# Kernel tuning notes

Measured on AMD Instinct MI355X. Metric: run time of the kernel, lower is better.

Reference implementation:

```python
import jax, jax.numpy as jnp
import numpy as np

B, L, C, H, FF = 2, 2048, 1024, 16, 4096
HD = C // H
SCALE = HD ** -0.5
EPS = 1e-5


def _ln(x, g, b):
    m = jnp.mean(x, axis=-1, keepdims=True)
    v = jnp.mean((x - m) ** 2, axis=-1, keepdims=True)
    return (x - m) * jax.lax.rsqrt(v + EPS) * g + b


def setup_inputs() -> dict:
    key = jax.random.key(0)
    ks = jax.random.split(key, 12)
    s = lambda fan_in: 1.0 / np.sqrt(fan_in)
    return {
        "x": jax.random.normal(ks[0], (B, L, C), jnp.float32),
        "freq_diff": jax.random.normal(ks[1], (B, L), jnp.float32),
        "qkv_w": jax.random.normal(ks[2], (C, 3 * C), jnp.float32) * s(C),
        "qkv_b": jnp.zeros((3 * C,), jnp.float32),
        "fp_w1": jax.random.normal(ks[3], (1, C), jnp.float32),
        "fp_b1": jnp.zeros((C,), jnp.float32),
        "fp_ln_g": jnp.ones((C,), jnp.float32),
        "fp_ln_b": jnp.zeros((C,), jnp.float32),
        "fp_w2": jax.random.normal(ks[4], (C, C), jnp.float32) * s(C),
        "fp_b2": jnp.zeros((C,), jnp.float32),
        "wq_w": jax.random.normal(ks[5], (HD, HD), jnp.float32) * s(HD),
        "wq_b": jnp.zeros((HD,), jnp.float32),
        "wk_w": jax.random.normal(ks[6], (HD, HD), jnp.float32) * s(HD),
        "wk_b": jnp.zeros((HD,), jnp.float32),
        "out_w": jax.random.normal(ks[7], (C, C), jnp.float32) * s(C),
        "out_b": jnp.zeros((C,), jnp.float32),
        "n1_g": jnp.ones((C,), jnp.float32),
        "n1_b": jnp.zeros((C,), jnp.float32),
        "n2_g": jnp.ones((C,), jnp.float32),
        "n2_b": jnp.zeros((C,), jnp.float32),
        "mlp_w1": jax.random.normal(ks[8], (C, FF), jnp.float32) * s(C),
        "mlp_b1": jnp.zeros((FF,), jnp.float32),
        "mlp_w2": jax.random.normal(ks[9], (FF, C), jnp.float32) * s(FF),
        "mlp_b2": jnp.zeros((C,), jnp.float32),
        "freq_scale": jnp.ones((1,), jnp.float32),
    }


def reference(x, freq_diff, qkv_w, qkv_b, fp_w1, fp_b1, fp_ln_g, fp_ln_b,
              fp_w2, fp_b2, wq_w, wq_b, wk_w, wk_b, out_w, out_b,
              n1_g, n1_b, n2_g, n2_b, mlp_w1, mlp_b1, mlp_w2, mlp_b2,
              freq_scale):
    shortcut = x
    xn = _ln(x, n1_g, n1_b)
    qkv = (xn @ qkv_w + qkv_b).reshape(B, L, 3, H, HD)
    qkv = jnp.transpose(qkv, (2, 0, 3, 1, 4))  # [3,B,H,L,HD]
    q, k, v = qkv[0], qkv[1], qkv[2]

    # frequency bias: MLP on scalar freq_diff -> per-head bias vectors
    fb = freq_diff[..., None] @ fp_w1 + fp_b1          # [B,L,C]
    fb = jax.nn.gelu(_ln(fb, fp_ln_g, fp_ln_b), approximate=False)
    fb = fb @ fp_w2 + fp_b2                            # [B,L,C]
    fb = jnp.transpose(fb.reshape(B, L, H, HD), (0, 2, 1, 3))  # [B,H,L,HD]
    qb = fb @ wq_w + wq_b
    kb = fb @ wk_w + wk_b
    freq_attn_bias = jnp.einsum('bhqd,bhkd->bhqk', qb, kb)

    attn = jnp.einsum('bhqd,bhkd->bhqk', q, k) * SCALE
    attn = attn + freq_scale[0] * freq_attn_bias
    attn = jax.nn.softmax(attn, axis=-1)
    o = jnp.einsum('bhqk,bhkd->bhqd', attn, v)
    o = jnp.transpose(o, (0, 2, 1, 3)).reshape(B, L, C)
    x = shortcut + (o @ out_w + out_b)

    xn2 = _ln(x, n2_g, n2_b)
    h = jax.nn.gelu(xn2 @ mlp_w1 + mlp_b1, approximate=False)
    x = x + (h @ mlp_w2 + mlp_b2)
    return x
```

## Files before the change

### kernel.cpp

```cpp
#include <hip/hip_runtime.h>
#include <math.h>


typedef __bf16 bf16;
typedef float f32x4 __attribute__((ext_vector_type(4)));
typedef bf16 bf16x8 __attribute__((ext_vector_type(8)));
typedef bf16 bf16x4 __attribute__((ext_vector_type(4)));

#define DEVINL __device__ __forceinline__

#define LOG2E 1.4426950408889634f

DEVINL float fast_exp2(float x) { return __builtin_amdgcn_exp2f(x); }

DEVINL void async_load16(const void* g, void* l) {
  __builtin_amdgcn_global_load_lds(
      (const __attribute__((address_space(1))) unsigned int*)g,
      (__attribute__((address_space(3))) unsigned int*)l, 16, 0, 0);
}

DEVINL f32x4 mfma16(bf16x8 a, bf16x8 b, f32x4 c) {
  return __builtin_amdgcn_mfma_f32_16x16x32_bf16(a, b, c, 0, 0, 0);
}

DEVINL float gelu_exact(float v) {
  return 0.5f * v * (1.0f + erff(v * 0.70710678118654752f));
}

DEVINL void hard_barrier() {
  asm volatile("" ::: "memory");
  __builtin_amdgcn_s_barrier();
  asm volatile("" ::: "memory");
}

DEVINL void block_reduce2(float& a, float& b, float* red, int tid) {
#pragma unroll
  for (int off = 32; off >= 1; off >>= 1) {
    a += __shfl_xor(a, off);
    b += __shfl_xor(b, off);
  }
  int w = tid >> 6;
  if ((tid & 63) == 0) { red[2 * w] = a; red[2 * w + 1] = b; }
  __syncthreads();
  a = red[0] + red[2] + red[4] + red[6];
  b = red[1] + red[3] + red[5] + red[7];
  __syncthreads();
}

__global__ __launch_bounds__(256) void pre_kernel(
    const float* __restrict__ qkv_w, const float* __restrict__ out_w,
    const float* __restrict__ mlp_w1, const float* __restrict__ mlp_w2,
    bf16* __restrict__ qkv_wt, bf16* __restrict__ out_wt,
    bf16* __restrict__ w1t, bf16* __restrict__ w2t,
    const float* __restrict__ x, const float* __restrict__ fd,
    const float* __restrict__ g1, const float* __restrict__ b1,
    const float* __restrict__ fw1, const float* __restrict__ fb1,
    const float* __restrict__ flg, const float* __restrict__ flb,
    bf16* __restrict__ xn, bf16* __restrict__ gout) {
  __shared__ float tile[32][33];
  __shared__ float red[8];
  const int id = blockIdx.x, t = threadIdx.x;
  if (id < 12288) {
    const float* W; bf16* Wt; int K, N, bx, by;
    if (id < 3072) {
      W = qkv_w; Wt = qkv_wt; K = 1024; N = 3072; bx = id % 96; by = id / 96;
    } else if (id < 4096) {
      int i = id - 3072;
      W = out_w; Wt = out_wt; K = 1024; N = 1024; bx = i & 31; by = i >> 5;
    } else if (id < 8192) {
      int i = id - 4096;
      W = mlp_w1; Wt = w1t; K = 1024; N = 4096; bx = i & 127; by = i >> 7;
    } else {
      int i = id - 8192;
      W = mlp_w2; Wt = w2t; K = 4096; N = 1024; bx = i & 31; by = i >> 5;
    }
    int n0 = bx * 32, k0 = by * 32;
    int tx = t & 31, ty = t >> 5;
#pragma unroll
    for (int r = 0; r < 4; ++r)
      tile[ty + r * 8][tx] = W[(size_t)(k0 + ty + r * 8) * N + n0 + tx];
    __syncthreads();
#pragma unroll
    for (int r = 0; r < 4; ++r)
      Wt[(size_t)(n0 + ty + r * 8) * K + k0 + tx] = (bf16)tile[tx][ty + r * 8];
    return;
  }
  int tok = id - 12288;
  float4 xv = ((const float4*)(x + (size_t)tok * 1024))[t];
  float s = xv.x + xv.y + xv.z + xv.w;
  float ss = xv.x * xv.x + xv.y * xv.y + xv.z * xv.z + xv.w * xv.w;
  block_reduce2(s, ss, red, t);
  float mean = s * (1.0f / 1024.0f);
  float rsig = rsqrtf(ss * (1.0f / 1024.0f) - mean * mean + 1e-5f);
  float4 g4 = ((const float4*)g1)[t], b4 = ((const float4*)b1)[t];
  bf16x4 o;
  o[0] = (bf16)((xv.x - mean) * rsig * g4.x + b4.x);
  o[1] = (bf16)((xv.y - mean) * rsig * g4.y + b4.y);
  o[2] = (bf16)((xv.z - mean) * rsig * g4.z + b4.z);
  o[3] = (bf16)((xv.w - mean) * rsig * g4.w + b4.w);
  ((bf16x4*)xn)[(size_t)tok * 256 + t] = o;

  float dv = fd[tok];
  float4 w4 = ((const float4*)fw1)[t], c4 = ((const float4*)fb1)[t];
  float f0 = dv * w4.x + c4.x, f1 = dv * w4.y + c4.y;
  float f2 = dv * w4.z + c4.z, f3 = dv * w4.w + c4.w;
  s = f0 + f1 + f2 + f3;
  ss = f0 * f0 + f1 * f1 + f2 * f2 + f3 * f3;
  block_reduce2(s, ss, red, t);
  mean = s * (1.0f / 1024.0f);
  rsig = rsqrtf(ss * (1.0f / 1024.0f) - mean * mean + 1e-5f);
  float4 lg = ((const float4*)flg)[t], lb = ((const float4*)flb)[t];
  bf16x4 q;
  q[0] = (bf16)gelu_exact((f0 - mean) * rsig * lg.x + lb.x);
  q[1] = (bf16)gelu_exact((f1 - mean) * rsig * lg.y + lb.y);
  q[2] = (bf16)gelu_exact((f2 - mean) * rsig * lg.z + lb.z);
  q[3] = (bf16)gelu_exact((f3 - mean) * rsig * lg.w + lb.w);
  ((bf16x4*)gout)[(size_t)tok * 256 + t] = q;
}

__global__ __launch_bounds__(256) void prec_qk(
    const float* __restrict__ fp_w2, const float* __restrict__ fp_b2,
    const float* __restrict__ wq_w, const float* __restrict__ wq_b,
    const float* __restrict__ wk_w, const float* __restrict__ wk_b,
    bf16* __restrict__ wqk2t, float* __restrict__ bqk) {
  __shared__ float Wl[64 * 64];
  __shared__ float Al[64 * 128];
  const int id = blockIdx.x;
  const int sel = id >> 7, h = (id >> 3) & 15, ck = id & 7;
  const int t = threadIdx.x;
  const float* wsel = sel ? wk_w : wq_w;
#pragma unroll
  for (int i = 0; i < 4; ++i)
    ((float4*)Wl)[i * 256 + t] = ((const float4*)wsel)[i * 256 + t];
  const int c0 = ck * 128, off = h * 64;
#pragma unroll
  for (int it = 0; it < 8; ++it) {
    int idx = it * 256 + t;
    int rr = idx >> 4, c4 = idx & 15;
    float4 v = *(const float4*)(fp_w2 + (size_t)(c0 + rr) * 1024 + off + c4 * 4);
    float vv[4] = {v.x, v.y, v.z, v.w};
#pragma unroll
    for (int k = 0; k < 4; ++k) {
      int i2 = c4 * 4 + k;
      Al[i2 * 128 + (rr ^ (i2 & 31))] = vv[k];
    }
  }
  __syncthreads();
  const int cr = t & 127, jh = (t >> 7) * 32;
  float acc[32];
#pragma unroll
  for (int j = 0; j < 32; ++j) acc[j] = 0.f;
  for (int i = 0; i < 64; ++i) {
    float a = Al[i * 128 + (cr ^ (i & 31))];
    const float4* wrow = (const float4*)(Wl + i * 64 + jh);
#pragma unroll
    for (int j4 = 0; j4 < 8; ++j4) {
      float4 wv = wrow[j4];
      acc[j4 * 4 + 0] += a * wv.x;
      acc[j4 * 4 + 1] += a * wv.y;
      acc[j4 * 4 + 2] += a * wv.z;
      acc[j4 * 4 + 3] += a * wv.w;
    }
  }
  const int nbase = sel * 1024 + off + jh;
#pragma unroll
  for (int j = 0; j < 32; ++j)
    wqk2t[(size_t)(nbase + j) * 1024 + c0 + cr] = (bf16)acc[j];
  if (ck == 0 && t < 64) {
    float s = 0.f;
    for (int i = 0; i < 64; ++i) s += fp_b2[off + i] * Wl[i * 64 + t];
    bqk[sel * 1024 + off + t] = s + (sel ? wk_b[t] : wq_b[t]);
  }
}

__global__ __launch_bounds__(256) void ln_kernel(
    const float* __restrict__ xin, const float* __restrict__ g,
    const float* __restrict__ b, bf16* __restrict__ xout) {
  __shared__ float red[8];
  int tok = blockIdx.x, t = threadIdx.x;
  float4 xv = ((const float4*)(xin + (size_t)tok * 1024))[t];
  float s = xv.x + xv.y + xv.z + xv.w;
  float ss = xv.x * xv.x + xv.y * xv.y + xv.z * xv.z + xv.w * xv.w;
  block_reduce2(s, ss, red, t);
  float mean = s * (1.0f / 1024.0f);
  float rsig = rsqrtf(ss * (1.0f / 1024.0f) - mean * mean + 1e-5f);
  float4 g4 = ((const float4*)g)[t], b4 = ((const float4*)b)[t];
  bf16x4 o;
  o[0] = (bf16)((xv.x - mean) * rsig * g4.x + b4.x);
  o[1] = (bf16)((xv.y - mean) * rsig * g4.y + b4.y);
  o[2] = (bf16)((xv.z - mean) * rsig * g4.z + b4.z);
  o[3] = (bf16)((xv.w - mean) * rsig * g4.w + b4.w);
  ((bf16x4*)xout)[(size_t)tok * 256 + t] = o;
}

#define PHASE(MH, NH, LA, LB, STAGE_STMT, WAIT_STMT)                          \
  do {                                                                        \
    if (LA) {                                                                 \
      _Pragma("unroll") for (int ml = 0; ml < 4; ++ml) {                      \
        _Pragma("unroll") for (int ks = 0; ks < 2; ++ks) {                    \
          const int rr = ml * 16 + lm;                                        \
          const int cc = (((ks * 4 + quad) ^ (lm & 7)) << 3);                 \
          af[ml][ks] = *(const bf16x8*)&As[bsel][MH][wm][rr][cc];             \
        }                                                                     \
      }                                                                       \
    }                                                                         \
    if (LB) {                                                                 \
      _Pragma("unroll") for (int nl = 0; nl < 2; ++nl) {                      \
        _Pragma("unroll") for (int ks = 0; ks < 2; ++ks) {                    \
          const int rr = nl * 16 + lm;                                        \
          const int cc = (((ks * 4 + quad) ^ (lm & 7)) << 3);                 \
          bfr[nl][ks] = *(const bf16x8*)&Bs[bsel][NH][wn][rr][cc];            \
        }                                                                     \
      }                                                                       \
    }                                                                         \
    STAGE_STMT;                                                               \
    WAIT_STMT;                                                                \
    hard_barrier();                                                           \
    __builtin_amdgcn_s_setprio(1);                                            \
    _Pragma("unroll") for (int ks = 0; ks < 2; ++ks) {                        \
      _Pragma("unroll") for (int ml = 0; ml < 4; ++ml) {                      \
        _Pragma("unroll") for (int nl = 0; nl < 2; ++nl) {                    \
          acc[(MH)*4 + ml][(NH)*2 + nl] = mfma16(                             \
              af[ml][ks], bfr[nl][ks], acc[(MH)*4 + ml][(NH)*2 + nl]);        \
        }                                                                     \
      }                                                                       \
    }                                                                         \
    __builtin_amdgcn_s_setprio(0);                                            \
  } while (0)

template <class Epi>
__global__ __launch_bounds__(512, 2) void gemm256(
    const bf16* __restrict__ A, const bf16* __restrict__ Bt,
    int lda, int ldb, int K, int kstride, int nbx, int nblk, int rowoffz,
    Epi epi) {
  __shared__ __align__(16) bf16 As[2][2][2][64][64];
  __shared__ __align__(16) bf16 Bs[2][2][4][32][64];

  const int tid = threadIdx.x;
  const int lane = tid & 63, w = tid >> 6;
  const int quad = lane >> 4, lm = lane & 15;
  const int wm = w >> 2, wn = w & 3;

  const int kz = blockIdx.x / nblk;
  const int bid = blockIdx.x - kz * nblk;
  const int swz = (nblk & 7) ? bid : ((bid & 7) * (nblk >> 3) + (bid >> 3));
  const int tm = swz / nbx, tn = swz - tm * nbx;
  const int m0 = tm << 8, n0 = tn << 8;
  const int rowoff = kz * rowoffz;
  A += (size_t)kz * kstride;
  Bt += (size_t)kz * kstride;

  const bf16* Abase = A + (size_t)m0 * lda;
  const bf16* Bbase = Bt + (size_t)n0 * ldb;

  auto stageA = [&](int b, int mh, int kt) {
#pragma unroll
    for (int j = 0; j < 2; ++j) {
      const int q = (w * 2 + j) * 64 + lane;
      const int wm2 = q >> 9, rr = (q >> 3) & 63, c = q & 7;
      async_load16(Abase + (size_t)(wm2 * 128 + mh * 64 + rr) * lda +
                       (size_t)kt * 64 + ((c ^ (rr & 7)) << 3),
                   (char*)&As[b][mh][0][0][0] + (w * 2 + j) * 1024);
    }
  };
  auto stageB = [&](int b, int nh, int kt) {
#pragma unroll
    for (int j = 0; j < 2; ++j) {
      const int q = (w * 2 + j) * 64 + lane;
      const int wn4 = q >> 8, rr = (q >> 3) & 31, c = q & 7;
      async_load16(Bbase + (size_t)(wn4 * 64 + nh * 32 + rr) * ldb +
                       (size_t)kt * 64 + ((c ^ (rr & 7)) << 3),
                   (char*)&Bs[b][nh][0][0][0] + (w * 2 + j) * 1024);
    }
  };

  f32x4 acc[8][4];
#pragma unroll
  for (int i = 0; i < 8; ++i)
#pragma unroll
    for (int j = 0; j < 4; ++j) {
      acc[i][j][0] = 0.f; acc[i][j][1] = 0.f;
      acc[i][j][2] = 0.f; acc[i][j][3] = 0.f;
    }
  bf16x8 af[4][2], bfr[2][2];

  stageA(0, 0, 0);
  stageB(0, 1, 0);
  stageA(0, 1, 0);
  stageB(0, 0, 0);
  stageA(1, 0, 1);
  stageB(1, 1, 1);
  asm volatile("s_waitcnt vmcnt(4)" ::: "memory");
  hard_barrier();

  const int nt = K >> 6;
  int bsel = 0;
  for (int t = 0; t < nt; ++t, bsel ^= 1) {
    PHASE(0, 0, 1, 1, { if (t + 1 < nt) stageA(bsel ^ 1, 1, t + 1); }, {});
    PHASE(0, 1, 0, 1, { if (t + 1 < nt) stageB(bsel ^ 1, 0, t + 1); }, {});
    PHASE(1, 1, 1, 0, { if (t + 2 < nt) stageA(bsel, 0, t + 2); }, {});
    PHASE(1, 0, 0, 1, { if (t + 2 < nt) stageB(bsel, 1, t + 2); },
          {
            if (t + 2 < nt) {
              asm volatile("s_waitcnt vmcnt(4)" ::: "memory");
            } else if (t + 1 < nt) {
              asm volatile("s_waitcnt vmcnt(0)" ::: "memory");
            }
          });
  }

#pragma unroll
  for (int mi = 0; mi < 8; ++mi)
#pragma unroll
    for (int ni = 0; ni < 4; ++ni)
      epi(rowoff + m0 + wm * 128 + mi * 16 + quad * 4,
          n0 + wn * 64 + ni * 16 + lm, acc[mi][ni]);
}

template <class Epi>
__global__ __launch_bounds__(256) void gemm_bf16_k(
    const bf16* __restrict__ A, const bf16* __restrict__ Bt,
    int M, int N, int K, Epi epi) {
  __shared__ bf16 As[2][128 * 32];
  __shared__ bf16 Bs[2][128 * 32];
  const int tid = threadIdx.x;
  const int lane = tid & 63, w = tid >> 6;
  const int quad = lane >> 4, lm = lane & 15;
  const int wm = w >> 1, wn = w & 1;
  const int m0 = blockIdx.y * 128, n0 = blockIdx.x * 128;

  f32x4 acc[4][4];
#pragma unroll
  for (int i = 0; i < 4; ++i)
#pragma unroll
    for (int j = 0; j < 4; ++j) {
      acc[i][j][0] = 0.f; acc[i][j][1] = 0.f; acc[i][j][2] = 0.f; acc[i][j][3] = 0.f;
    }

  const bf16* Ag = A + (size_t)m0 * K;
  const bf16* Bg = Bt + (size_t)n0 * K;

  auto stage = [&](int k0, int buf) {
#pragma unroll
    for (int i = 0; i < 2; ++i) {
      int ch = i * 256 + tid, r = ch >> 2, c = ch & 3;
      async_load16(Ag + (size_t)r * K + k0 + c * 8,
                   (char*)As[buf] + (i * 256 + w * 64) * 16);
      async_load16(Bg + (size_t)r * K + k0 + c * 8,
                   (char*)Bs[buf] + (i * 256 + w * 64) * 16);
    }
  };

  stage(0, 0);
  const int nk = K >> 5;
  for (int ki = 0; ki < nk; ++ki) {
    __syncthreads();
    if (ki + 1 < nk) stage((ki + 1) << 5, (ki + 1) & 1);
    const bf16* Ac = As[ki & 1];
    const bf16* Bc = Bs[ki & 1];
    bf16x8 af[4], bfv[4];
#pragma unroll
    for (int mi = 0; mi < 4; ++mi)
      af[mi] = *(const bf16x8*)(Ac + (wm * 64 + mi * 16 + lm) * 32 + quad * 8);
#pragma unroll
    for (int ni = 0; ni < 4; ++ni)
      bfv[ni] = *(const bf16x8*)(Bc + (wn * 64 + ni * 16 + lm) * 32 + quad * 8);
#pragma unroll
    for (int mi = 0; mi < 4; ++mi)
#pragma unroll
      for (int ni = 0; ni < 4; ++ni)
        acc[mi][ni] = mfma16(af[mi], bfv[ni], acc[mi][ni]);
  }

#pragma unroll
  for (int mi = 0; mi < 4; ++mi)
#pragma unroll
    for (int ni = 0; ni < 4; ++ni)
      epi(m0 + wm * 64 + mi * 16 + quad * 4, n0 + wn * 64 + ni * 16 + lm, acc[mi][ni]);
}

__global__ __launch_bounds__(256) void reduce_mlp2(
    const float* __restrict__ part, float* __restrict__ out) {
  size_t i = (size_t)blockIdx.x * 256 + threadIdx.x;
  const float4* p = (const float4*)part;
  float4 o = ((const float4*)out)[i];
  const size_t S = (size_t)4096 * 256;
  float4 a = p[i], b = p[i + S], c = p[i + 2 * S], d = p[i + 3 * S];
  o.x += a.x + b.x + c.x + d.x;
  o.y += a.y + b.y + c.y + d.y;
  o.z += a.z + b.z + c.z + d.z;
  o.w += a.w + b.w + c.w + d.w;
  ((float4*)out)[i] = o;
}

struct EpiQKV {
  const float* __restrict__ bias;
  bf16 *Qc, *Kc, *Vt;
  DEVINL void operator()(int row, int col, f32x4 v) const {
    int b = row >> 11, l = row & 2047;
    float bia = bias[col];
    if (col < 1024) {
      int h = col >> 6, d = col & 63;
      bf16* p = Qc + (size_t)(((b << 4) + h) * 2048 + l) * 128 + d;
#pragma unroll
      for (int r = 0; r < 4; ++r) p[r * 128] = (bf16)((v[r] + bia) * (0.125f * LOG2E));
    } else if (col < 2048) {
      int c2 = col - 1024, h = c2 >> 6, d = c2 & 63;
      bf16* p = Kc + (size_t)(((b << 4) + h) * 2048 + l) * 128 + d;
#pragma unroll
      for (int r = 0; r < 4; ++r) p[r * 128] = (bf16)(v[r] + bia);
    } else {
      int c2 = col - 2048, h = c2 >> 6, d = c2 & 63;
      bf16x4 pk;
#pragma unroll
      for (int r = 0; r < 4; ++r) pk[r] = (bf16)(v[r] + bia);
      *(bf16x4*)(Vt + (size_t)(((b << 4) + h) * 64 + d) * 2048 + l) = pk;
    }
  }
};

struct EpiQBKB {
  const float* __restrict__ bias;
  const float* __restrict__ fs;
  bf16 *Qc, *Kc;
  DEVINL void operator()(int row, int col, f32x4 v) const {
    int b = row >> 11, l = row & 2047;
    float bia = bias[col];
    if (col < 1024) {
      int h = col >> 6, d = col & 63;
      float sc = fs[0] * LOG2E;
      bf16* p = Qc + (size_t)(((b << 4) + h) * 2048 + l) * 128 + 64 + d;
#pragma unroll
      for (int r = 0; r < 4; ++r) p[r * 128] = (bf16)((v[r] + bia) * sc);
    } else {
      int c2 = col - 1024, h = c2 >> 6, d = c2 & 63;
      bf16* p = Kc + (size_t)(((b << 4) + h) * 2048 + l) * 128 + 64 + d;
#pragma unroll
      for (int r = 0; r < 4; ++r) p[r * 128] = (bf16)(v[r] + bia);
    }
  }
};

struct EpiOut {
  const float* __restrict__ bias;
  const float* __restrict__ x;
  const float* __restrict__ b2;
  float* x1;
  float* out0;
  DEVINL void operator()(int row, int col, f32x4 v) const {
    float bia = bias[col];
    float b2v = b2[col];
#pragma unroll
    for (int r = 0; r < 4; ++r) {
      size_t idx = (size_t)(row + r) * 1024 + col;
      float xv = x[idx] + v[r] + bia;
      x1[idx] = xv;
      out0[idx] = xv + b2v;
    }
  }
};

struct EpiMLP1 {
  const float* __restrict__ bias;
  bf16* hbf;
  DEVINL void operator()(int row, int col, f32x4 v) const {
    float bia = bias[col];
#pragma unroll
    for (int r = 0; r < 4; ++r)
      hbf[(size_t)(row + r) * 4096 + col] = (bf16)gelu_exact(v[r] + bia);
  }
};

struct EpiPart {
  float* part;
  DEVINL void operator()(int row, int col, f32x4 v) const {
#pragma unroll
    for (int r = 0; r < 4; ++r)
      part[(size_t)(row + r) * 1024 + col] = v[r];
  }
};

__global__ __launch_bounds__(512, 4) void flash_kernel(
    const bf16* __restrict__ Qc, const bf16* __restrict__ Kcp,
    const bf16* __restrict__ Vt, bf16* __restrict__ Obf) {
  __shared__ bf16 KsA[64 * 128];
  __shared__ bf16 KsB[64 * 128];
  __shared__ bf16 VsA[64 * 64];
  __shared__ bf16 VsB[64 * 64];
  __shared__ bf16 Ps[128 * 64];

  const int tid = threadIdx.x, lane = tid & 63, w = tid >> 6;
  const int quad = lane >> 4, lm = lane & 15;
  const int id = blockIdx.x;
  const int bh = id & 31, qt = id >> 5;
  const int b = bh >> 4, h = bh & 15;

  const bf16* Qg = Qc + ((size_t)bh * 2048 + qt * 128) * 128;
#pragma unroll
  for (int i = 0; i < 4; ++i) {
    int ch = i * 512 + tid, r = ch >> 4, cs = ch & 15, c = cs ^ (r & 7);
    char* dst = (i < 2) ? (char*)KsA + (i * 512 + w * 64) * 16
                        : (char*)KsB + ((i - 2) * 512 + w * 64) * 16;
    async_load16(Qg + (size_t)r * 128 + c * 8, dst);
  }
  __syncthreads();
  const int qr = w * 16 + lm;
  bf16x8 qf[4];
  {
    const bf16* base = (w < 4) ? KsA : KsB;
    int rr = qr & 63;
#pragma unroll
    for (int ks = 0; ks < 4; ++ks) {
      int pos = (ks * 4 + quad) ^ (lm & 7);
      qf[ks] = *(const bf16x8*)(base + rr * 128 + pos * 8);
    }
  }
  __syncthreads();

  float m_run = -3.0e38f, l_lane = 0.f;
  f32x4 o_acc[4];
#pragma unroll
  for (int nf = 0; nf < 4; ++nf) {
    o_acc[nf][0] = 0.f; o_acc[nf][1] = 0.f; o_acc[nf][2] = 0.f; o_acc[nf][3] = 0.f;
  }

  const bf16* Kg0 = Kcp + (size_t)bh * 2048 * 128;
  const bf16* Vg0 = Vt + (size_t)bh * 64 * 2048;

  auto stage = [&](int kv, bf16* Kdst, bf16* Vdst) {
    const bf16* Kg = Kg0 + (size_t)kv * 64 * 128;
#pragma unroll
    for (int i = 0; i < 2; ++i) {
      int ch = i * 512 + tid, key = ch >> 4, c = (ch & 15) ^ (key & 7);
      async_load16(Kg + (size_t)key * 128 + c * 8,
                   (char*)Kdst + (i * 512 + w * 64) * 16);
    }
    {
      int d = tid >> 3, c = (tid & 7) ^ (d & 7);
      async_load16(Vg0 + (size_t)d * 2048 + kv * 64 + c * 8,
                   (char*)Vdst + (w * 64) * 16);
    }
  };

  stage(0, KsA, VsA);

  for (int kv = 0; kv < 32; ++kv) {
    const bf16* Kcur = (kv & 1) ? KsB : KsA;
    const bf16* Vcur = (kv & 1) ? VsB : VsA;
    __syncthreads();
    if (kv + 1 < 32)
      stage(kv + 1, (kv & 1) ? KsA : KsB, (kv & 1) ? VsA : VsB);

    f32x4 sa[4];
#pragma unroll
    for (int nk = 0; nk < 4; ++nk) {
      sa[nk][0] = 0.f; sa[nk][1] = 0.f; sa[nk][2] = 0.f; sa[nk][3] = 0.f;
    }
#pragma unroll
    for (int ks = 0; ks < 4; ++ks) {
      bf16x8 ak[4];
#pragma unroll
      for (int nk = 0; nk < 4; ++nk) {
        int key = nk * 16 + lm;
        int pos = (ks * 4 + quad) ^ (key & 7);
        ak[nk] = *(const bf16x8*)(Kcur + key * 128 + pos * 8);
      }
#pragma unroll
      for (int nk = 0; nk < 4; ++nk)
        sa[nk] = mfma16(ak[nk], qf[ks], sa[nk]);
    }

    float mx = fmaxf(fmaxf(sa[0][0], sa[0][1]), sa[0][2]);
    mx = fmaxf(fmaxf(mx, sa[0][3]), sa[1][0]);
    mx = fmaxf(fmaxf(mx, sa[1][1]), sa[1][2]);
    mx = fmaxf(fmaxf(mx, sa[1][3]), sa[2][0]);
    mx = fmaxf(fmaxf(mx, sa[2][1]), sa[2][2]);
    mx = fmaxf(fmaxf(mx, sa[2][3]), sa[3][0]);
    mx = fmaxf(fmaxf(mx, sa[3][1]), sa[3][2]);
    mx = fmaxf(mx, sa[3][3]);
    mx = fmaxf(mx, __shfl_xor(mx, 16));
    mx = fmaxf(mx, __shfl_xor(mx, 32));
    if (__any(mx > m_run + 8.0f)) {
      float mnew = fmaxf(m_run, mx);
      float alpha = fast_exp2(m_run - mnew);
      m_run = mnew;
      l_lane *= alpha;
#pragma unroll
      for (int nf = 0; nf < 4; ++nf) {
        o_acc[nf][0] *= alpha; o_acc[nf][1] *= alpha;
        o_acc[nf][2] *= alpha; o_acc[nf][3] *= alpha;
      }
    }
    float rs = 0.f;
#pragma unroll
    for (int nk = 0; nk < 4; ++nk)
#pragma unroll
      for (int rg = 0; rg < 4; ++rg) {
        float pv = fast_exp2(sa[nk][rg] - m_run);
        sa[nk][rg] = pv;
        rs += pv;
      }
    l_lane += rs;

#pragma unroll
    for (int nk = 0; nk < 4; ++nk) {
      int c16 = 2 * nk + (quad >> 1);
      int cs = c16 ^ (lm & 7);
      bf16x4 pk;
      pk[0] = (bf16)sa[nk][0]; pk[1] = (bf16)sa[nk][1];
      pk[2] = (bf16)sa[nk][2]; pk[3] = (bf16)sa[nk][3];
      *(bf16x4*)(Ps + qr * 64 + cs * 8 + (quad & 1) * 4) = pk;
    }

#pragma unroll
    for (int ks = 0; ks < 2; ++ks) {
      bf16x8 pa, vb[4];
      {
        int cs = (ks * 4 + quad) ^ (lm & 7);
        pa = *(const bf16x8*)(Ps + qr * 64 + cs * 8);
      }
#pragma unroll
      for (int nf = 0; nf < 4; ++nf) {
        int d = nf * 16 + lm;
        int cs = (ks * 4 + quad) ^ (d & 7);
        vb[nf] = *(const bf16x8*)(Vcur + d * 64 + cs * 8);
      }
#pragma unroll
      for (int nf = 0; nf < 4; ++nf)
        o_acc[nf] = mfma16(vb[nf], pa, o_acc[nf]);
    }
  }

  float lt = l_lane;
  lt += __shfl_xor(lt, 16);
  lt += __shfl_xor(lt, 32);
  float inv = 1.0f / lt;
  int l = qt * 128 + qr;
#pragma unroll
  for (int nf = 0; nf < 4; ++nf) {
    bf16x4 ov;
#pragma unroll
    for (int rg = 0; rg < 4; ++rg) ov[rg] = (bf16)(o_acc[nf][rg] * inv);
    int d = h * 64 + nf * 16 + quad * 4;
    *(bf16x4*)(Obf + ((size_t)b * 2048 + l) * 1024 + d) = ov;
  }
}

extern "C" void kernel_launch(void* const* d_in, const int* in_sizes, int n_in,
                              void* d_out, int out_size, void* d_ws, size_t ws_size,
                              hipStream_t stream) {
  (void)in_sizes; (void)n_in; (void)out_size; (void)ws_size;
  const float* x      = (const float*)d_in[0];
  const float* fd     = (const float*)d_in[1];
  const float* qkv_w  = (const float*)d_in[2];
  const float* qkv_b  = (const float*)d_in[3];
  const float* fp_w1  = (const float*)d_in[4];
  const float* fp_b1  = (const float*)d_in[5];
  const float* fp_ln_g= (const float*)d_in[6];
  const float* fp_ln_b= (const float*)d_in[7];
  const float* fp_w2  = (const float*)d_in[8];
  const float* fp_b2  = (const float*)d_in[9];
  const float* wq_w   = (const float*)d_in[10];
  const float* wq_b   = (const float*)d_in[11];
  const float* wk_w   = (const float*)d_in[12];
  const float* wk_b   = (const float*)d_in[13];
  const float* out_w  = (const float*)d_in[14];
  const float* out_b  = (const float*)d_in[15];
  const float* n1_g   = (const float*)d_in[16];
  const float* n1_b   = (const float*)d_in[17];
  const float* n2_g   = (const float*)d_in[18];
  const float* n2_b   = (const float*)d_in[19];
  const float* mlp_w1 = (const float*)d_in[20];
  const float* mlp_b1 = (const float*)d_in[21];
  const float* mlp_w2 = (const float*)d_in[22];
  const float* mlp_b2 = (const float*)d_in[23];
  const float* fscale = (const float*)d_in[24];
  float* out = (float*)d_out;

  char* p = (char*)d_ws;
  auto take = [&](size_t n) { char* r = p; p += (n + 255) & ~(size_t)255; return r; };
  bf16* xn_bf  = (bf16*)take((size_t)4096 * 1024 * 2);
  bf16* g_bf   = (bf16*)take((size_t)4096 * 1024 * 2);
  bf16* Qc     = (bf16*)take((size_t)32 * 2048 * 128 * 2);
  bf16* Kc     = (bf16*)take((size_t)32 * 2048 * 128 * 2);
  bf16* Vt     = (bf16*)take((size_t)32 * 64 * 2048 * 2);
  bf16* o_bf   = (bf16*)take((size_t)4096 * 1024 * 2);
  float* x1    = (float*)take((size_t)4096 * 1024 * 4);
  bf16* ln2_bf = (bf16*)take((size_t)4096 * 1024 * 2);
  bf16* h_bf   = (bf16*)take((size_t)4096 * 4096 * 2);
  bf16* qkv_wt = (bf16*)take((size_t)3072 * 1024 * 2);
  bf16* out_wt = (bf16*)take((size_t)1024 * 1024 * 2);
  bf16* w1t    = (bf16*)take((size_t)4096 * 1024 * 2);
  bf16* w2t    = (bf16*)take((size_t)1024 * 4096 * 2);
  bf16* wqk2t  = (bf16*)take((size_t)2048 * 1024 * 2);
  float* bqk   = (float*)take((size_t)2048 * 4);

  float* part = (float*)xn_bf;

  dim3 b256(256), b512(512);

  prec_qk<<<dim3(256), b256, 0, stream>>>(fp_w2, fp_b2, wq_w, wq_b, wk_w, wk_b, wqk2t, bqk);
  pre_kernel<<<dim3(16384), b256, 0, stream>>>(
      qkv_w, out_w, mlp_w1, mlp_w2, qkv_wt, out_wt, w1t, w2t,
      x, fd, n1_g, n1_b, fp_w1, fp_b1, fp_ln_g, fp_ln_b, xn_bf, g_bf);

  gemm256<<<dim3(192), b512, 0, stream>>>(xn_bf, qkv_wt, 1024, 1024, 1024, 0,
                                          12, 192, 0, EpiQKV{qkv_b, Qc, Kc, Vt});
  gemm256<<<dim3(128), b512, 0, stream>>>(g_bf, wqk2t, 1024, 1024, 1024, 0,
                                          8, 128, 0, EpiQBKB{bqk, fscale, Qc, Kc});
  flash_kernel<<<dim3(512), dim3(512), 0, stream>>>(Qc, Kc, Vt, o_bf);

  gemm_bf16_k<<<dim3(8, 32), b256, 0, stream>>>(o_bf, out_wt, 4096, 1024, 1024,
                                                EpiOut{out_b, x, mlp_b2, x1, out});
  ln_kernel<<<dim3(4096), b256, 0, stream>>>(x1, n2_g, n2_b, ln2_bf);
  gemm256<<<dim3(256), b512, 0, stream>>>(ln2_bf, w1t, 1024, 1024, 1024, 0,
                                          16, 256, 0, EpiMLP1{mlp_b1, h_bf});
  gemm256<<<dim3(256), b512, 0, stream>>>(h_bf, w2t, 4096, 4096, 1024, 1024,
                                          4, 64, 4096, EpiPart{part});
  reduce_mlp2<<<dim3(4096), b256, 0, stream>>>(part, out);
}
```

Measured before the change: 460.8 us.

## Split-K out-proj with gemm256, fuse residual+LN2 reduce, load V directly to registers

The output projection moves from the small 128x128 gemm to the larger gemm256 kernel using a two-way split-K into a partial buffer that reuses the h_bf workspace. A new reduce_oln kernel sums the partials with the residual and bias, writes out0, and computes LayerNorm2 in one pass, replacing the separate epilogue and ln_kernel and dropping the x1 buffer. Separately, the flash kernel stops staging V through LDS and loads V fragments straight from global memory into registers. This cuts LDS use and a pass over memory, at the cost of extra partial-buffer traffic and uncoalesced, unhidden V loads inside the attention loop.

```diff
diff --git a/kernel.cpp b/kernel.cpp
--- a/kernel.cpp
+++ b/kernel.cpp
@@ -173,24 +173,39 @@
   }
 }
 
-__global__ __launch_bounds__(256) void ln_kernel(
-    const float* __restrict__ xin, const float* __restrict__ g,
-    const float* __restrict__ b, bf16* __restrict__ xout) {
+__global__ __launch_bounds__(256) void reduce_oln(
+    const float* __restrict__ part, const float* __restrict__ x,
+    const float* __restrict__ outb, const float* __restrict__ b2,
+    const float* __restrict__ g, const float* __restrict__ bb,
+    float* __restrict__ out0, bf16* __restrict__ ln2) {
   __shared__ float red[8];
   int tok = blockIdx.x, t = threadIdx.x;
-  float4 xv = ((const float4*)(xin + (size_t)tok * 1024))[t];
-  float s = xv.x + xv.y + xv.z + xv.w;
-  float ss = xv.x * xv.x + xv.y * xv.y + xv.z * xv.z + xv.w * xv.w;
+  size_t base = (size_t)tok * 256 + t;
+  const size_t S = (size_t)4096 * 256;
+  float4 p0 = ((const float4*)part)[base];
+  float4 p1 = ((const float4*)part)[base + S];
+  float4 xv = ((const float4*)x)[base];
+  float4 ob = ((const float4*)outb)[t];
+  float v0 = xv.x + p0.x + p1.x + ob.x;
+  float v1 = xv.y + p0.y + p1.y + ob.y;
+  float v2 = xv.z + p0.z + p1.z + ob.z;
+  float v3 = xv.w + p0.w + p1.w + ob.w;
+  float s = v0 + v1 + v2 + v3;
+  float ss = v0 * v0 + v1 * v1 + v2 * v2 + v3 * v3;
   block_reduce2(s, ss, red, t);
   float mean = s * (1.0f / 1024.0f);
   float rsig = rsqrtf(ss * (1.0f / 1024.0f) - mean * mean + 1e-5f);
-  float4 g4 = ((const float4*)g)[t], b4 = ((const float4*)b)[t];
+  float4 g4 = ((const float4*)g)[t], bb4 = ((const float4*)bb)[t];
   bf16x4 o;
-  o[0] = (bf16)((xv.x - mean) * rsig * g4.x + b4.x);
-  o[1] = (bf16)((xv.y - mean) * rsig * g4.y + b4.y);
-  o[2] = (bf16)((xv.z - mean) * rsig * g4.z + b4.z);
-  o[3] = (bf16)((xv.w - mean) * rsig * g4.w + b4.w);
-  ((bf16x4*)xout)[(size_t)tok * 256 + t] = o;
+  o[0] = (bf16)((v0 - mean) * rsig * g4.x + bb4.x);
+  o[1] = (bf16)((v1 - mean) * rsig * g4.y + bb4.y);
+  o[2] = (bf16)((v2 - mean) * rsig * g4.z + bb4.z);
+  o[3] = (bf16)((v3 - mean) * rsig * g4.w + bb4.w);
+  ((bf16x4*)ln2)[base] = o;
+  float4 b24 = ((const float4*)b2)[t];
+  float4 ov;
+  ov.x = v0 + b24.x; ov.y = v1 + b24.y; ov.z = v2 + b24.z; ov.w = v3 + b24.w;
+  ((float4*)out0)[base] = ov;
 }
 
 #define PHASE(MH, NH, LA, LB, STAGE_STMT, WAIT_STMT)                          \
@@ -317,68 +332,6 @@
           n0 + wn * 64 + ni * 16 + lm, acc[mi][ni]);
 }
 
-template <class Epi>
-__global__ __launch_bounds__(256) void gemm_bf16_k(
-    const bf16* __restrict__ A, const bf16* __restrict__ Bt,
-    int M, int N, int K, Epi epi) {
-  __shared__ bf16 As[2][128 * 32];
-  __shared__ bf16 Bs[2][128 * 32];
-  const int tid = threadIdx.x;
-  const int lane = tid & 63, w = tid >> 6;
-  const int quad = lane >> 4, lm = lane & 15;
-  const int wm = w >> 1, wn = w & 1;
-  const int m0 = blockIdx.y * 128, n0 = blockIdx.x * 128;
-
-  f32x4 acc[4][4];
-#pragma unroll
-  for (int i = 0; i < 4; ++i)
-#pragma unroll
-    for (int j = 0; j < 4; ++j) {
-      acc[i][j][0] = 0.f; acc[i][j][1] = 0.f; acc[i][j][2] = 0.f; acc[i][j][3] = 0.f;
-    }
-
-  const bf16* Ag = A + (size_t)m0 * K;
-  const bf16* Bg = Bt + (size_t)n0 * K;
-
-  auto stage = [&](int k0, int buf) {
-#pragma unroll
-    for (int i = 0; i < 2; ++i) {
-      int ch = i * 256 + tid, r = ch >> 2, c = ch & 3;
-      async_load16(Ag + (size_t)r * K + k0 + c * 8,
-                   (char*)As[buf] + (i * 256 + w * 64) * 16);
-      async_load16(Bg + (size_t)r * K + k0 + c * 8,
-                   (char*)Bs[buf] + (i * 256 + w * 64) * 16);
-    }
-  };
-
-  stage(0, 0);
-  const int nk = K >> 5;
-  for (int ki = 0; ki < nk; ++ki) {
-    __syncthreads();
-    if (ki + 1 < nk) stage((ki + 1) << 5, (ki + 1) & 1);
-    const bf16* Ac = As[ki & 1];
-    const bf16* Bc = Bs[ki & 1];
-    bf16x8 af[4], bfv[4];
-#pragma unroll
-    for (int mi = 0; mi < 4; ++mi)
-      af[mi] = *(const bf16x8*)(Ac + (wm * 64 + mi * 16 + lm) * 32 + quad * 8);
-#pragma unroll
-    for (int ni = 0; ni < 4; ++ni)
-      bfv[ni] = *(const bf16x8*)(Bc + (wn * 64 + ni * 16 + lm) * 32 + quad * 8);
-#pragma unroll
-    for (int mi = 0; mi < 4; ++mi)
-#pragma unroll
-      for (int ni = 0; ni < 4; ++ni)
-        acc[mi][ni] = mfma16(af[mi], bfv[ni], acc[mi][ni]);
-  }
-
-#pragma unroll
-  for (int mi = 0; mi < 4; ++mi)
-#pragma unroll
-    for (int ni = 0; ni < 4; ++ni)
-      epi(m0 + wm * 64 + mi * 16 + quad * 4, n0 + wn * 64 + ni * 16 + lm, acc[mi][ni]);
-}
-
 __global__ __launch_bounds__(256) void reduce_mlp2(
     const float* __restrict__ part, float* __restrict__ out) {
   size_t i = (size_t)blockIdx.x * 256 + threadIdx.x;
@@ -441,25 +394,6 @@
   }
 };
 
-struct EpiOut {
-  const float* __restrict__ bias;
-  const float* __restrict__ x;
-  const float* __restrict__ b2;
-  float* x1;
-  float* out0;
-  DEVINL void operator()(int row, int col, f32x4 v) const {
-    float bia = bias[col];
-    float b2v = b2[col];
-#pragma unroll
-    for (int r = 0; r < 4; ++r) {
-      size_t idx = (size_t)(row + r) * 1024 + col;
-      float xv = x[idx] + v[r] + bia;
-      x1[idx] = xv;
-      out0[idx] = xv + b2v;
-    }
-  }
-};
-
 struct EpiMLP1 {
   const float* __restrict__ bias;
   bf16* hbf;
@@ -485,8 +419,6 @@
     const bf16* __restrict__ Vt, bf16* __restrict__ Obf) {
   __shared__ bf16 KsA[64 * 128];
   __shared__ bf16 KsB[64 * 128];
-  __shared__ bf16 VsA[64 * 64];
-  __shared__ bf16 VsB[64 * 64];
   __shared__ bf16 Ps[128 * 64];
 
   const int tid = threadIdx.x, lane = tid & 63, w = tid >> 6;
@@ -527,7 +459,7 @@
   const bf16* Kg0 = Kcp + (size_t)bh * 2048 * 128;
   const bf16* Vg0 = Vt + (size_t)bh * 64 * 2048;
 
-  auto stage = [&](int kv, bf16* Kdst, bf16* Vdst) {
+  auto stageK = [&](int kv, bf16* Kdst) {
     const bf16* Kg = Kg0 + (size_t)kv * 64 * 128;
 #pragma unroll
     for (int i = 0; i < 2; ++i) {
@@ -535,21 +467,23 @@
       async_load16(Kg + (size_t)key * 128 + c * 8,
                    (char*)Kdst + (i * 512 + w * 64) * 16);
     }
-    {
-      int d = tid >> 3, c = (tid & 7) ^ (d & 7);
-      async_load16(Vg0 + (size_t)d * 2048 + kv * 64 + c * 8,
-                   (char*)Vdst + (w * 64) * 16);
-    }
   };
 
-  stage(0, KsA, VsA);
+  stageK(0, KsA);
 
   for (int kv = 0; kv < 32; ++kv) {
     const bf16* Kcur = (kv & 1) ? KsB : KsA;
-    const bf16* Vcur = (kv & 1) ? VsB : VsA;
     __syncthreads();
-    if (kv + 1 < 32)
-      stage(kv + 1, (kv & 1) ? KsA : KsB, (kv & 1) ? VsA : VsB);
+    if (kv + 1 < 32) stageK(kv + 1, (kv & 1) ? KsA : KsB);
+
+    bf16x8 vg[2][4];
+    const bf16* Vg = Vg0 + kv * 64;
+#pragma unroll
+    for (int ks = 0; ks < 2; ++ks)
+#pragma unroll
+      for (int nf = 0; nf < 4; ++nf)
+        vg[ks][nf] = *(const bf16x8*)(Vg + (size_t)(nf * 16 + lm) * 2048 +
+                                      ks * 32 + quad * 8);
 
     f32x4 sa[4];
 #pragma unroll
@@ -614,20 +548,14 @@
 
 #pragma unroll
     for (int ks = 0; ks < 2; ++ks) {
-      bf16x8 pa, vb[4];
+      bf16x8 pa;
       {
         int cs = (ks * 4 + quad) ^ (lm & 7);
         pa = *(const bf16x8*)(Ps + qr * 64 + cs * 8);
       }
 #pragma unroll
-      for (int nf = 0; nf < 4; ++nf) {
-        int d = nf * 16 + lm;
-        int cs = (ks * 4 + quad) ^ (d & 7);
-        vb[nf] = *(const bf16x8*)(Vcur + d * 64 + cs * 8);
-      }
-#pragma unroll
       for (int nf = 0; nf < 4; ++nf)
-        o_acc[nf] = mfma16(vb[nf], pa, o_acc[nf]);
+        o_acc[nf] = mfma16(vg[ks][nf], pa, o_acc[nf]);
     }
   }
 
@@ -685,7 +613,6 @@
   bf16* Kc     = (bf16*)take((size_t)32 * 2048 * 128 * 2);
   bf16* Vt     = (bf16*)take((size_t)32 * 64 * 2048 * 2);
   bf16* o_bf   = (bf16*)take((size_t)4096 * 1024 * 2);
-  float* x1    = (float*)take((size_t)4096 * 1024 * 4);
   bf16* ln2_bf = (bf16*)take((size_t)4096 * 1024 * 2);
   bf16* h_bf   = (bf16*)take((size_t)4096 * 4096 * 2);
   bf16* qkv_wt = (bf16*)take((size_t)3072 * 1024 * 2);
@@ -696,6 +623,7 @@
   float* bqk   = (float*)take((size_t)2048 * 4);
 
   float* part = (float*)xn_bf;
+  float* opart = (float*)h_bf;
 
   dim3 b256(256), b512(512);
 
@@ -710,9 +638,10 @@
                                           8, 128, 0, EpiQBKB{bqk, fscale, Qc, Kc});
   flash_kernel<<<dim3(512), dim3(512), 0, stream>>>(Qc, Kc, Vt, o_bf);
 
-  gemm_bf16_k<<<dim3(8, 32), b256, 0, stream>>>(o_bf, out_wt, 4096, 1024, 1024,
-                                                EpiOut{out_b, x, mlp_b2, x1, out});
-  ln_kernel<<<dim3(4096), b256, 0, stream>>>(x1, n2_g, n2_b, ln2_bf);
+  gemm256<<<dim3(128), b512, 0, stream>>>(o_bf, out_wt, 1024, 1024, 512, 512,
+                                          4, 64, 4096, EpiPart{opart});
+  reduce_oln<<<dim3(4096), b256, 0, stream>>>(opart, x, out_b, mlp_b2,
+                                              n2_g, n2_b, out, ln2_bf);
   gemm256<<<dim3(256), b512, 0, stream>>>(ln2_bf, w1t, 1024, 1024, 1024, 0,
                                           16, 256, 0, EpiMLP1{mlp_b1, h_bf});
   gemm256<<<dim3(256), b512, 0, stream>>>(h_bf, w2t, 4096, 4096, 1024, 1024,
```

Measured after the change: 517.7 us. +12.3%, slower.
